# Kernel optimization log

Measured on AMD Instinct MI355X. Metric: run time of the kernel, lower is better.

Reference implementation:

```python
import jax, jax.numpy as jnp
import numpy as np
import math

VOCAB = 32000
D_MODEL = 512
N_LAYERS = 6
N_HEADS = 8
DIM_FF = 2048
B, L = 4, 2048
MAX_LEN = 5000
EPS = 1e-5


def _pos_encoding(max_len, d_model):
    pe = np.zeros((max_len, d_model), dtype=np.float32)
    pos = np.arange(max_len)[:, None].astype(np.float32)
    div = np.exp(np.arange(0, d_model, 2).astype(np.float32) * (-math.log(10000.0) / d_model))
    pe[:, 0::2] = np.sin(pos * div)
    pe[:, 1::2] = np.cos(pos * div)
    return jnp.asarray(pe)


def setup_inputs() -> dict:
    key = jax.random.key(0)
    ks = jax.random.split(key, 16)
    s = 0.02
    d, f, Ly = D_MODEL, DIM_FF, N_LAYERS
    inp = {
        "src": jax.random.randint(ks[0], (B, L), 0, VOCAB, dtype=jnp.int32),
        "embed": jax.random.normal(ks[1], (VOCAB, d), jnp.float32) * s,
        "pe": _pos_encoding(MAX_LEN, d),
        "Wq": jax.random.normal(ks[2], (Ly, d, d), jnp.float32) * s,
        "bq": jnp.zeros((Ly, d), jnp.float32),
        "Wk": jax.random.normal(ks[3], (Ly, d, d), jnp.float32) * s,
        "bk": jnp.zeros((Ly, d), jnp.float32),
        "Wv": jax.random.normal(ks[4], (Ly, d, d), jnp.float32) * s,
        "bv": jnp.zeros((Ly, d), jnp.float32),
        "Wo": jax.random.normal(ks[5], (Ly, d, d), jnp.float32) * s,
        "bo": jnp.zeros((Ly, d), jnp.float32),
        "W1": jax.random.normal(ks[6], (Ly, d, f), jnp.float32) * s,
        "b1": jnp.zeros((Ly, f), jnp.float32),
        "W2": jax.random.normal(ks[7], (Ly, f, d), jnp.float32) * s,
        "b2": jnp.zeros((Ly, d), jnp.float32),
        "g1": jnp.ones((Ly, d), jnp.float32),
        "be1": jnp.zeros((Ly, d), jnp.float32),
        "g2": jnp.ones((Ly, d), jnp.float32),
        "be2": jnp.zeros((Ly, d), jnp.float32),
    }
    return inp


def _layernorm(x, g, b):
    mu = jnp.mean(x, axis=-1, keepdims=True)
    var = jnp.mean((x - mu) ** 2, axis=-1, keepdims=True)
    return (x - mu) * jax.lax.rsqrt(var + EPS) * g + b


def _encoder(src, embed, pe, Wq, bq, Wk, bk, Wv, bv, Wo, bo, W1, b1, W2, b2, g1, be1, g2, be2):
    Bb, Ll = src.shape
    H = N_HEADS
    hd = D_MODEL // H
    x = embed[src] + pe[:Ll]  # [B, L, D]
    for i in range(Wq.shape[0]):
        # NOTE: faithful to the source: .view(B, H, L, hd) with NO transpose
        q = (x @ Wq[i] + bq[i]).reshape(Bb, H, Ll, hd)
        k = (x @ Wk[i] + bk[i]).reshape(Bb, H, Ll, hd)
        v = (x @ Wv[i] + bv[i]).reshape(Bb, H, Ll, hd)
        scores = jnp.einsum('bhqd,bhkd->bhqk', q, k) / math.sqrt(hd)
        w = jax.nn.softmax(scores, axis=-1)
        o = jnp.einsum('bhqk,bhkd->bhqd', w, v)
        o = o.transpose(0, 2, 1, 3).reshape(Bb, Ll, D_MODEL)
        o = o @ Wo[i] + bo[i]
        x = _layernorm(x + o, g1[i], be1[i])
        ff = jax.nn.relu(x @ W1[i] + b1[i]) @ W2[i] + b2[i]
        x = _layernorm(x + ff, g2[i], be2[i])
    return x


def reference(src, embed, pe, Wq, bq, Wk, bk, Wv, bv, Wo, bo, W1, b1, W2, b2, g1, be1, g2, be2):
    return _encoder(src, embed, pe, Wq, bq, Wk, bk, Wv, bv, Wo, bo, W1, b1, W2, b2, g1, be1, g2, be2)
```

## Files before the change

### kernel.cpp

```cpp
#include <hip/hip_runtime.h>
#include <hip/hip_bf16.h>

typedef unsigned short u16;
typedef __attribute__((ext_vector_type(8))) short bf16x8;
typedef __attribute__((ext_vector_type(2))) unsigned u32x2;
typedef __attribute__((ext_vector_type(4))) float f32x4;
typedef __attribute__((ext_vector_type(16))) float f32x16;

#define B_  4
#define L_  2048
#define D_  512
#define H_  8
#define HD_ 64
#define FF_ 2048
#define NL_ 6
#define M_  8192
#define MB_ 1048576ULL

#if __has_builtin(__builtin_amdgcn_exp2f)
#define EX2 __builtin_amdgcn_exp2f
#else
#define EX2 exp2f
#endif

__device__ __forceinline__ float b2f(u16 u) {
    unsigned v = ((unsigned)u) << 16;
    return __builtin_bit_cast(float, v);
}
__device__ __forceinline__ u16 f2b(float f) {
    unsigned u = __builtin_bit_cast(unsigned, f);
    unsigned r = u + 0x7FFFu + ((u >> 16) & 1u);
    return (u16)(r >> 16);
}
__device__ __forceinline__ unsigned pack2_bf16(float a, float b) {
    __hip_bfloat162 h = __float22bfloat162_rn(make_float2(a, b));
    unsigned u;
    __builtin_memcpy(&u, &h, 4);
    return u;
}
__device__ __forceinline__ float inp(const void* p, size_t i, int fp32) {
    return fp32 ? ((const float*)p)[i] : b2f(((const u16*)p)[i]);
}
__device__ __forceinline__ void gl2lds16(const void* g, void* l) {
    __builtin_amdgcn_global_load_lds(
        (const __attribute__((address_space(1))) void*)g,
        (__attribute__((address_space(3))) void*)l, 16, 0, 0);
}

__global__ void probe_k(const unsigned* __restrict__ g1, int* __restrict__ flag) {
    flag[0] = (g1[0] == 0x3F800000u) ? 1 : 0;
}

__global__ __launch_bounds__(256) void transpose_layer_k2(const void* __restrict__ Wq,
                                                          const void* __restrict__ Wk,
                                                          const void* __restrict__ Wv,
                                                          const void* __restrict__ Wo,
                                                          const void* __restrict__ W1,
                                                          const void* __restrict__ W2,
                                                          size_t wo, size_t wf,
                                                          u16* __restrict__ Wt,
                                                          const int* __restrict__ flag) {
    __shared__ u16 tile[32][33];
    int fp32 = flag[0];
    int bid = blockIdx.x;
    const void* in;
    size_t off;
    u16* out;
    int rows, cols, tx, ty;
    if (bid < 1024) {
        int which = bid >> 8;
        in = (which == 0) ? Wq : (which == 1) ? Wk : (which == 2) ? Wv : Wo;
        off = wo;
        out = Wt + (size_t)which * (512 * 512);
        rows = 512; cols = 512;
        int t = bid & 255; tx = t & 15; ty = t >> 4;
    } else if (bid < 2048) {
        in = W1; off = wf; out = Wt + 4 * (512 * 512);
        rows = 512; cols = 2048;
        int t = bid - 1024; tx = t & 63; ty = t >> 6;
    } else {
        in = W2; off = wf; out = Wt + 4 * (512 * 512) + 512 * 2048;
        rows = 2048; cols = 512;
        int t = bid - 2048; tx = t & 15; ty = t >> 4;
    }
    int c0 = tx * 32, r0 = ty * 32;
    int lx = threadIdx.x & 31, ly = threadIdx.x >> 5;
    #pragma unroll
    for (int i = ly; i < 32; i += 8)
        tile[i][lx] = f2b(inp(in, off + (size_t)(r0 + i) * cols + c0 + lx, fp32));
    __syncthreads();
    #pragma unroll
    for (int i = ly; i < 32; i += 8)
        out[(size_t)(c0 + i) * rows + r0 + lx] = tile[lx][i];
}

__global__ __launch_bounds__(256) void embed_k(const int* __restrict__ src,
                                               const void* __restrict__ embed,
                                               const void* __restrict__ pe,
                                               float* __restrict__ xf,
                                               u16* __restrict__ xb,
                                               const int* __restrict__ flag) {
    int fp32 = flag[0];
    int idx = blockIdx.x * 256 + threadIdx.x;
    int m = idx >> 9;
    int d = idx & 511;
    int tok = src[m];
    float v = inp(embed, (size_t)tok * D_ + d, fp32)
            + inp(pe, (size_t)(m & (L_ - 1)) * D_ + d, fp32);
    xf[idx] = v;
    xb[idx] = f2b(v);
}

template <int TM, int TN, int WM, int WN, int WRITE_BF16, int RELU>
__device__ __forceinline__ void gemm_core(const u16* __restrict__ A,
                                          const u16* __restrict__ Bt,
                                          int tnB, int tnC,
                                          const void* __restrict__ bias, size_t boff,
                                          float* __restrict__ Cf, u16* __restrict__ Cb,
                                          int N, int K, int kbeg, int kend,
                                          float cscale, int fp32, int use_bias) {
    constexpr int BK = 32;
    __shared__ u16 Asm[TM * BK];
    __shared__ u16 Bsm[TN * BK];
    int tm = blockIdx.y * TM;
    int tid = threadIdx.x;
    int wave = tid >> 6, lane = tid & 63, quad = lane >> 4, l16 = lane & 15;
    constexpr int NWN = TN / WN;
    int wm = (wave / NWN) * WM, wn = (wave % NWN) * WN;
    constexpr int FI = WM / 16, FJ = WN / 16;
    constexpr int CA = TM / 64;
    constexpr int CB = TN / 64;

    int arowl = (lane >> 2);
    int akc   = (lane & 3) * 8;

    f32x4 acc[FI][FJ];
    #pragma unroll
    for (int i = 0; i < FI; i++)
        #pragma unroll
        for (int j = 0; j < FJ; j++) { f32x4 z = {0.f, 0.f, 0.f, 0.f}; acc[i][j] = z; }

    for (int k0 = kbeg; k0 < kend; k0 += BK) {
        __syncthreads();
        #pragma unroll
        for (int c = 0; c < CA; c++) {
            int chunk = wave * CA + c;
            int row = chunk * 16 + arowl;
            gl2lds16(A + (size_t)(tm + row) * K + k0 + akc, &Asm[chunk * 16 * BK]);
        }
        #pragma unroll
        for (int c = 0; c < CB; c++) {
            int chunk = wave * CB + c;
            int row = chunk * 16 + arowl;
            gl2lds16(Bt + (size_t)(tnB + row) * K + k0 + akc, &Bsm[chunk * 16 * BK]);
        }
        __syncthreads();
        bf16x8 af[FI], bfr[FJ];
        #pragma unroll
        for (int i = 0; i < FI; i++)
            af[i] = *(bf16x8*)&Asm[(wm + i * 16 + l16) * BK + quad * 8];
        #pragma unroll
        for (int j = 0; j < FJ; j++)
            bfr[j] = *(bf16x8*)&Bsm[(wn + j * 16 + l16) * BK + quad * 8];
        #pragma unroll
        for (int i = 0; i < FI; i++)
            #pragma unroll
            for (int j = 0; j < FJ; j++)
                acc[i][j] = __builtin_amdgcn_mfma_f32_16x16x32_bf16(af[i], bfr[j], acc[i][j], 0, 0, 0);
    }

    #pragma unroll
    for (int i = 0; i < FI; i++) {
        int row = tm + wm + i * 16 + quad * 4;
        #pragma unroll
        for (int j = 0; j < FJ; j++) {
            int col = tnC + wn + j * 16 + l16;
            float bv = use_bias ? inp(bias, boff + col, fp32) : 0.f;
            #pragma unroll
            for (int r = 0; r < 4; r++) {
                float v = (acc[i][j][r] + bv) * cscale;
                if (RELU) v = v > 0.f ? v : 0.f;
                size_t idx = (size_t)(row + r) * N + col;
                if (WRITE_BF16) Cb[idx] = f2b(v);
                else            Cf[idx] = v;
            }
        }
    }
}

__global__ __launch_bounds__(256) void gemm_qkv(const u16* A, const u16* Wt,
                                                const void* bq, const void* bk, const void* bv,
                                                size_t boff, u16* Qb, u16* Kb, u16* Vb,
                                                int K, float qscale, const int* flag) {
    int tnB = blockIdx.x * 128;
    int mat = tnB >> 9;
    int tnC = tnB & 511;
    u16* Cb = (mat == 0) ? Qb : (mat == 1) ? Kb : Vb;
    const void* bias = (mat == 0) ? bq : (mat == 1) ? bk : bv;
    float sc = (mat == 0) ? qscale : 1.0f;
    gemm_core<128, 128, 64, 64, 1, 0>(A, Wt, tnB, tnC, bias, boff, nullptr, Cb, 512, K, 0, K, sc, flag[0], 1);
}
__global__ __launch_bounds__(256) void gemm128_b16_relu(const u16* A, const u16* Bt, const void* bias, size_t boff,
                                                        u16* Cb, int N, int K, const int* flag) {
    int tn = blockIdx.x * 128;
    gemm_core<128, 128, 64, 64, 1, 1>(A, Bt, tn, tn, bias, boff, nullptr, Cb, N, K, 0, K, 1.0f, flag[0], 1);
}
__global__ __launch_bounds__(256) void gemm64_f32_sk(const u16* A, const u16* Bt, const void* bias, size_t boff,
                                                     float* Cf, int N, int K, const int* flag) {
    int tn = blockIdx.x * 128;
    int z = blockIdx.z;
    int ks = K / gridDim.z;
    gemm_core<64, 128, 64, 32, 0, 0>(A, Bt, tn, tn, bias, boff, Cf + (size_t)z * M_ * 512, nullptr,
                                     N, K, z * ks, z * ks + ks, 1.0f, flag[0], z == 0);
}

__global__ __launch_bounds__(256) void vperm_k(const u16* __restrict__ in, u16* __restrict__ out) {
    __shared__ u16 tile[32][33];
    int bh = blockIdx.z;
    const u16* pin = in + (size_t)bh * (L_ * HD_);
    u16* pout = out + (size_t)bh * (L_ * HD_);
    int c0 = blockIdx.x * 32, r0 = blockIdx.y * 32;
    int lx = threadIdx.x & 31, ly = threadIdx.x >> 5;
    #pragma unroll
    for (int i = ly; i < 32; i += 8)
        tile[i][lx] = pin[(size_t)(r0 + i) * HD_ + c0 + lx];
    __syncthreads();
    #pragma unroll
    for (int i = ly; i < 32; i += 8)
        pout[(size_t)(c0 + i) * L_ + r0 + lx] = tile[lx][i];
}

__device__ __forceinline__ bf16x8 frag_from4(unsigned w0, unsigned w1, unsigned w2, unsigned w3) {
    union { unsigned u[4]; bf16x8 v; } t;
    t.u[0] = w0; t.u[1] = w1; t.u[2] = w2; t.u[3] = w3;
    return t.v;
}
__device__ __forceinline__ void lane32_swap(unsigned& x, unsigned& y, int hi) {
#if __has_builtin(__builtin_amdgcn_permlane32_swap)
    u32x2 r = __builtin_amdgcn_permlane32_swap(x, y, false, false);
    x = r[0]; y = r[1];
#else
    unsigned tx = (unsigned)__shfl_xor((int)x, 32, 64);
    unsigned ty = (unsigned)__shfl_xor((int)y, 32, 64);
    x = hi ? ty : x;
    y = hi ? y : tx;
#endif
}

__global__ __launch_bounds__(256, 4) void attn_k(const u16* __restrict__ Q,
                                                 const u16* __restrict__ K,
                                                 const u16* __restrict__ Vt,
                                                 u16* __restrict__ O) {
    constexpr int NT = L_ / 64;
    __shared__ u16 TILES[4][64 * 64];
    __shared__ float LsP[2][2][2][32];
    int qt = blockIdx.x;
    int bh = blockIdx.y;
    int b = bh >> 3, h = bh & 7;
    size_t hb = (size_t)bh * (L_ * HD_);
    int tid = threadIdx.x, wave = tid >> 6, lane = tid & 63, hi = lane >> 5, r32 = lane & 31;
    int wqq = wave >> 1, wk = wave & 1;

    const char* Kg = (const char*)(K + hb);
    const char* Vg = (const char*)(Vt + hb);

    int rsub = lane >> 3;
    int scol = (((lane & 7) ^ rsub) << 4);

    const u16* qp = Q + hb + (size_t)(qt * 64 + wqq * 32 + r32) * HD_ + hi * 8;
    bf16x8 qf[4];
    #pragma unroll
    for (int dc = 0; dc < 4; dc++) qf[dc] = *(const bf16x8*)(qp + dc * 16);

    #pragma unroll
    for (int c = 0; c < 2; c++) {
        int row = wave * 16 + c * 8 + rsub;
        gl2lds16(Kg + (size_t)row * (HD_ * 2) + scol, &TILES[0][(wave * 16 + c * 8) * 64]);
        gl2lds16(Vg + (size_t)row * (L_ * 2) + scol, &TILES[2][(wave * 16 + c * 8) * 64]);
    }

    f32x16 oac0, oac1;
    #pragma unroll
    for (int i = 0; i < 16; i++) { oac0[i] = 0.f; oac1[i] = 0.f; }
    float ls = 0.f;

    int krow = wk * 32 + r32;
    int ksw = (krow & 7) << 4;
    int vsw = (r32 & 7) << 4;

    int cur = 0;
    for (int kt = 0; kt < NT; kt++) {
        __syncthreads();
        if (kt + 1 < NT) {
            #pragma unroll
            for (int c = 0; c < 2; c++) {
                int row = wave * 16 + c * 8 + rsub;
                gl2lds16(Kg + (size_t)((kt + 1) * 64 + row) * (HD_ * 2) + scol,
                         &TILES[cur ^ 1][(wave * 16 + c * 8) * 64]);
                gl2lds16(Vg + (size_t)row * (L_ * 2) + (kt + 1) * 128 + scol,
                         &TILES[2 + (cur ^ 1)][(wave * 16 + c * 8) * 64]);
            }
        }

        const char* Kb = (const char*)&TILES[cur][0];
        const char* Vb = (const char*)&TILES[2 + cur][0];

        bf16x8 kf[4];
        #pragma unroll
        for (int dc = 0; dc < 4; dc++)
            kf[dc] = *(const bf16x8*)(Kb + krow * 128 + ((dc * 32 + hi * 16) ^ ksw));
        bf16x8 vf[4];
        vf[0] = *(const bf16x8*)(Vb + r32 * 128        + ((wk * 64 + hi * 16) ^ vsw));
        vf[1] = *(const bf16x8*)(Vb + r32 * 128        + ((wk * 64 + 32 + hi * 16) ^ vsw));
        vf[2] = *(const bf16x8*)(Vb + (32 + r32) * 128 + ((wk * 64 + hi * 16) ^ vsw));
        vf[3] = *(const bf16x8*)(Vb + (32 + r32) * 128 + ((wk * 64 + 32 + hi * 16) ^ vsw));

        f32x16 sac;
        #pragma unroll
        for (int i = 0; i < 16; i++) sac[i] = 0.f;
        __builtin_amdgcn_s_setprio(1);
        #pragma unroll
        for (int dc = 0; dc < 4; dc++)
            sac = __builtin_amdgcn_mfma_f32_32x32x16_bf16(kf[dc], qf[dc], sac, 0, 0, 0);
        __builtin_amdgcn_s_setprio(0);

        float p[16];
        #pragma unroll
        for (int r = 0; r < 16; r++) p[r] = EX2(sac[r]);
        {
            float a = (p[0] + p[1]) + (p[2] + p[3]);
            float c = (p[4] + p[5]) + (p[6] + p[7]);
            float e = (p[8] + p[9]) + (p[10] + p[11]);
            float g = (p[12] + p[13]) + (p[14] + p[15]);
            ls += (a + c) + (e + g);
        }
        bf16x8 pa[2];
        #pragma unroll
        for (int c = 0; c < 2; c++) {
            int rb = c * 8;
            unsigned a0 = pack2_bf16(p[rb + 0], p[rb + 1]);
            unsigned a1 = pack2_bf16(p[rb + 2], p[rb + 3]);
            unsigned a2 = pack2_bf16(p[rb + 4], p[rb + 5]);
            unsigned a3 = pack2_bf16(p[rb + 6], p[rb + 7]);
            lane32_swap(a0, a2, hi);
            lane32_swap(a1, a3, hi);
            pa[c] = frag_from4(a0, a1, a2, a3);
        }

        __builtin_amdgcn_s_setprio(1);
        oac0 = __builtin_amdgcn_mfma_f32_32x32x16_bf16(pa[0], vf[0], oac0, 0, 0, 0);
        oac1 = __builtin_amdgcn_mfma_f32_32x32x16_bf16(pa[0], vf[2], oac1, 0, 0, 0);
        oac0 = __builtin_amdgcn_mfma_f32_32x32x16_bf16(pa[1], vf[1], oac0, 0, 0, 0);
        oac1 = __builtin_amdgcn_mfma_f32_32x32x16_bf16(pa[1], vf[3], oac1, 0, 0, 0);
        __builtin_amdgcn_s_setprio(0);

        cur ^= 1;
    }

    __syncthreads();
    float* RedF = (float*)&TILES[0][0];
    LsP[wqq][wk][hi][r32] = ls;
    if (wk == 1) {
        #pragma unroll
        for (int r = 0; r < 16; r++) {
            RedF[(wqq * 64 + lane) * 33 + r]      = oac0[r];
            RedF[(wqq * 64 + lane) * 33 + 16 + r] = oac1[r];
        }
    }
    __syncthreads();
    if (wk == 0) {
        #pragma unroll
        for (int r = 0; r < 16; r++) {
            int qr = (r & 3) + 8 * (r >> 2) + 4 * hi;
            float den = LsP[wqq][0][0][qr] + LsP[wqq][0][1][qr]
                      + LsP[wqq][1][0][qr] + LsP[wqq][1][1][qr];
            float inv = 1.0f / fmaxf(den, 1e-30f);
            float v0 = (oac0[r] + RedF[(wqq * 64 + lane) * 33 + r]) * inv;
            float v1 = (oac1[r] + RedF[(wqq * 64 + lane) * 33 + 16 + r]) * inv;
            int qg = qt * 64 + wqq * 32 + qr;
            size_t ob = ((size_t)b * L_ + qg) * D_ + h * HD_;
            O[ob + r32]      = f2b(v0);
            O[ob + 32 + r32] = f2b(v1);
        }
    }
}

__global__ __launch_bounds__(256) void ln_k2(const float* resid,
                                             const float* __restrict__ delta0,
                                             const float* __restrict__ delta1,
                                             const void* __restrict__ g,
                                             const void* __restrict__ be, size_t goff,
                                             float* xf_out,
                                             void* __restrict__ out_raw,
                                             const int* __restrict__ flag,
                                             int two, int is_final) {
    int fp32 = flag[0];
    int row = blockIdx.x * 4 + (threadIdx.x >> 6);
    int lane = threadIdx.x & 63;
    const float* pr = resid + (size_t)row * D_;
    const float* pd0 = delta0 + (size_t)row * D_;
    const float* pd1 = delta1 + (size_t)row * D_;
    float u[8];
    float s = 0.f;
    #pragma unroll
    for (int i = 0; i < 8; i++) {
        int c = lane + i * 64;
        u[i] = pr[c] + pd0[c] + (two ? pd1[c] : 0.f);
        s += u[i];
    }
    #pragma unroll
    for (int d = 1; d < 64; d <<= 1) s += __shfl_xor(s, d);
    float mu = s * (1.0f / 512.0f);
    float vs = 0.f;
    #pragma unroll
    for (int i = 0; i < 8; i++) { float t = u[i] - mu; vs += t * t; }
    #pragma unroll
    for (int d = 1; d < 64; d <<= 1) vs += __shfl_xor(vs, d);
    float rstd = rsqrtf(vs * (1.0f / 512.0f) + 1e-5f);
    #pragma unroll
    for (int i = 0; i < 8; i++) {
        int c = lane + i * 64;
        float v = (u[i] - mu) * rstd * inp(g, goff + c, fp32) + inp(be, goff + c, fp32);
        xf_out[(size_t)row * D_ + c] = v;
        size_t oi = (size_t)row * D_ + c;
        if (is_final && fp32) ((float*)out_raw)[oi] = v;
        else                  ((u16*)out_raw)[oi]  = f2b(v);
    }
}

extern "C" void kernel_launch(void* const* d_in, const int* in_sizes, int n_in,
                              void* d_out, int out_size, void* d_ws, size_t ws_size,
                              hipStream_t stream) {
    (void)in_sizes; (void)n_in; (void)out_size;
    const int*  src   = (const int*)d_in[0];
    const void* embed = d_in[1];
    const void* pe    = d_in[2];
    const void* Wq = d_in[3];  const void* bq = d_in[4];
    const void* Wk = d_in[5];  const void* bk = d_in[6];
    const void* Wv = d_in[7];  const void* bv = d_in[8];
    const void* Wo = d_in[9];  const void* bo = d_in[10];
    const void* W1 = d_in[11]; const void* b1 = d_in[12];
    const void* W2 = d_in[13]; const void* b2 = d_in[14];
    const void* g1 = d_in[15]; const void* be1 = d_in[16];
    const void* g2 = d_in[17]; const void* be2 = d_in[18];

    int big = (ws_size >= 103 * MB_ + 64);
    char* ws = (char*)d_ws;
    float* xf  = (float*)(ws);
    u16*  xb   = (u16*)(ws + 16 * MB_);
    u16*  Qb   = (u16*)(ws + 24 * MB_);
    u16*  Kb   = (u16*)(ws + 32 * MB_);
    u16*  Vb   = (u16*)(ws + 40 * MB_);
    u16*  Vt   = (u16*)(ws + 48 * MB_);
    u16*  Ab   = (u16*)(ws + 56 * MB_);
    float* Pf0 = (float*)(ws + 24 * MB_);
    float* Pf1 = (float*)(ws + 40 * MB_);
    u16*  Hb   = (u16*)(ws + (big ? 64 : 40) * MB_);
    u16*  Wt   = (u16*)(ws + (big ? 96 : 72) * MB_);
    int*  flag = (int*)(ws + (big ? 102 : 78) * MB_);
    u16* Wot = Wt + 786432;
    u16* W1t = Wt + 1048576;
    u16* W2t = Wt + 2097152;

    const float QSCALE = 0.125f * 1.44269504f;

    probe_k<<<1, 1, 0, stream>>>((const unsigned*)g1, flag);
    embed_k<<<(M_ * D_) / 256, 256, 0, stream>>>(src, embed, pe, xf, xb, flag);

    for (int i = 0; i < NL_; i++) {
        size_t wo = (size_t)i * 512 * 512;
        size_t wf = (size_t)i * 512 * 2048;
        size_t vo = (size_t)i * 512;
        size_t fo = (size_t)i * 2048;
        transpose_layer_k2<<<3072, 256, 0, stream>>>(Wq, Wk, Wv, Wo, W1, W2, wo, wf, Wt, flag);

        gemm_qkv<<<dim3(12, 64), 256, 0, stream>>>(xb, Wt, bq, bk, bv, vo, Qb, Kb, Vb, 512, QSCALE, flag);
        vperm_k<<<dim3(2, 64, 32), 256, 0, stream>>>(Vb, Vt);
        attn_k<<<dim3(32, 32), 256, 0, stream>>>(Qb, Kb, Vt, Ab);
        gemm64_f32_sk<<<dim3(4, 128, 1), 256, 0, stream>>>(Ab, Wot, bo, vo, Pf0, 512, 512, flag);
        ln_k2<<<M_ / 4, 256, 0, stream>>>(xf, Pf0, Pf0, g1, be1, vo, xf, xb, flag, 0, 0);
        gemm128_b16_relu<<<dim3(16, 64), 256, 0, stream>>>(xb, W1t, b1, fo, Hb, 2048, 512, flag);
        if (big) gemm64_f32_sk<<<dim3(4, 128, 2), 256, 0, stream>>>(Hb, W2t, b2, vo, Pf0, 512, 2048, flag);
        else     gemm64_f32_sk<<<dim3(4, 128, 1), 256, 0, stream>>>(Hb, W2t, b2, vo, Pf0, 512, 2048, flag);
        void* out_raw = (i == NL_ - 1) ? d_out : (void*)xb;
        ln_k2<<<M_ / 4, 256, 0, stream>>>(xf, Pf0, Pf1, g2, be2, vo, xf, out_raw, flag, big ? 1 : 0, (i == NL_ - 1) ? 1 : 0);
    }
}
```

Before: 1.391 ms.

## Widen GEMM K-step to 64 and use 128-query attention blocks with 8 waves

The GEMM core now loads two 32-wide K slices per barrier pair, halving the number of __syncthreads per K loop at the cost of doubled LDS. The attention kernel grows to 512 threads covering 128 query rows per block, so each K/V tile staged in LDS is shared by twice as many queries and each wave loads half as many rows. Attention also gets a dedicated reduction buffer instead of reusing the tile memory, which raises LDS use and may lower occupancy.

```diff
diff --git a/kernel.cpp b/kernel.cpp
--- a/kernel.cpp
+++ b/kernel.cpp
@@ -120,8 +120,8 @@
                                           int N, int K, int kbeg, int kend,
                                           float cscale, int fp32, int use_bias) {
     constexpr int BK = 32;
-    __shared__ u16 Asm[TM * BK];
-    __shared__ u16 Bsm[TN * BK];
+    __shared__ u16 Asm[2][TM * BK];
+    __shared__ u16 Bsm[2][TN * BK];
     int tm = blockIdx.y * TM;
     int tid = threadIdx.x;
     int wave = tid >> 6, lane = tid & 63, quad = lane >> 4, l16 = lane & 15;
@@ -140,33 +140,40 @@
         #pragma unroll
         for (int j = 0; j < FJ; j++) { f32x4 z = {0.f, 0.f, 0.f, 0.f}; acc[i][j] = z; }
 
-    for (int k0 = kbeg; k0 < kend; k0 += BK) {
+    for (int k0 = kbeg; k0 < kend; k0 += 64) {
         __syncthreads();
         #pragma unroll
-        for (int c = 0; c < CA; c++) {
-            int chunk = wave * CA + c;
-            int row = chunk * 16 + arowl;
-            gl2lds16(A + (size_t)(tm + row) * K + k0 + akc, &Asm[chunk * 16 * BK]);
-        }
-        #pragma unroll
-        for (int c = 0; c < CB; c++) {
-            int chunk = wave * CB + c;
-            int row = chunk * 16 + arowl;
-            gl2lds16(Bt + (size_t)(tnB + row) * K + k0 + akc, &Bsm[chunk * 16 * BK]);
+        for (int half = 0; half < 2; half++) {
+            int kh = k0 + half * 32;
+            #pragma unroll
+            for (int c = 0; c < CA; c++) {
+                int chunk = wave * CA + c;
+                int row = chunk * 16 + arowl;
+                gl2lds16(A + (size_t)(tm + row) * K + kh + akc, &Asm[half][chunk * 16 * BK]);
+            }
+            #pragma unroll
+            for (int c = 0; c < CB; c++) {
+                int chunk = wave * CB + c;
+                int row = chunk * 16 + arowl;
+                gl2lds16(Bt + (size_t)(tnB + row) * K + kh + akc, &Bsm[half][chunk * 16 * BK]);
+            }
         }
         __syncthreads();
-        bf16x8 af[FI], bfr[FJ];
-        #pragma unroll
-        for (int i = 0; i < FI; i++)
-            af[i] = *(bf16x8*)&Asm[(wm + i * 16 + l16) * BK + quad * 8];
-        #pragma unroll
-        for (int j = 0; j < FJ; j++)
-            bfr[j] = *(bf16x8*)&Bsm[(wn + j * 16 + l16) * BK + quad * 8];
-        #pragma unroll
-        for (int i = 0; i < FI; i++)
+        #pragma unroll
+        for (int half = 0; half < 2; half++) {
+            bf16x8 af[FI], bfr[FJ];
+            #pragma unroll
+            for (int i = 0; i < FI; i++)
+                af[i] = *(bf16x8*)&Asm[half][(wm + i * 16 + l16) * BK + quad * 8];
             #pragma unroll
             for (int j = 0; j < FJ; j++)
-                acc[i][j] = __builtin_amdgcn_mfma_f32_16x16x32_bf16(af[i], bfr[j], acc[i][j], 0, 0, 0);
+                bfr[j] = *(bf16x8*)&Bsm[half][(wn + j * 16 + l16) * BK + quad * 8];
+            #pragma unroll
+            for (int i = 0; i < FI; i++)
+                #pragma unroll
+                for (int j = 0; j < FJ; j++)
+                    acc[i][j] = __builtin_amdgcn_mfma_f32_16x16x32_bf16(af[i], bfr[j], acc[i][j], 0, 0, 0);
+        }
     }
 
     #pragma unroll
@@ -247,13 +254,14 @@
 #endif
 }
 
-__global__ __launch_bounds__(256, 4) void attn_k(const u16* __restrict__ Q,
+__global__ __launch_bounds__(512, 4) void attn_k(const u16* __restrict__ Q,
                                                  const u16* __restrict__ K,
                                                  const u16* __restrict__ Vt,
                                                  u16* __restrict__ O) {
     constexpr int NT = L_ / 64;
     __shared__ u16 TILES[4][64 * 64];
-    __shared__ float LsP[2][2][2][32];
+    __shared__ float RedF[4][64][33];
+    __shared__ float LsP[4][2][2][32];
     int qt = blockIdx.x;
     int bh = blockIdx.y;
     int b = bh >> 3, h = bh & 7;
@@ -266,18 +274,15 @@
 
     int rsub = lane >> 3;
     int scol = (((lane & 7) ^ rsub) << 4);
-
-    const u16* qp = Q + hb + (size_t)(qt * 64 + wqq * 32 + r32) * HD_ + hi * 8;
+    int srow = wave * 8 + rsub;
+
+    const u16* qp = Q + hb + (size_t)(qt * 128 + wqq * 32 + r32) * HD_ + hi * 8;
     bf16x8 qf[4];
     #pragma unroll
     for (int dc = 0; dc < 4; dc++) qf[dc] = *(const bf16x8*)(qp + dc * 16);
 
-    #pragma unroll
-    for (int c = 0; c < 2; c++) {
-        int row = wave * 16 + c * 8 + rsub;
-        gl2lds16(Kg + (size_t)row * (HD_ * 2) + scol, &TILES[0][(wave * 16 + c * 8) * 64]);
-        gl2lds16(Vg + (size_t)row * (L_ * 2) + scol, &TILES[2][(wave * 16 + c * 8) * 64]);
-    }
+    gl2lds16(Kg + (size_t)srow * (HD_ * 2) + scol, &TILES[0][(wave * 8) * 64]);
+    gl2lds16(Vg + (size_t)srow * (L_ * 2) + scol, &TILES[2][(wave * 8) * 64]);
 
     f32x16 oac0, oac1;
     #pragma unroll
@@ -292,14 +297,10 @@
     for (int kt = 0; kt < NT; kt++) {
         __syncthreads();
         if (kt + 1 < NT) {
-            #pragma unroll
-            for (int c = 0; c < 2; c++) {
-                int row = wave * 16 + c * 8 + rsub;
-                gl2lds16(Kg + (size_t)((kt + 1) * 64 + row) * (HD_ * 2) + scol,
-                         &TILES[cur ^ 1][(wave * 16 + c * 8) * 64]);
-                gl2lds16(Vg + (size_t)row * (L_ * 2) + (kt + 1) * 128 + scol,
-                         &TILES[2 + (cur ^ 1)][(wave * 16 + c * 8) * 64]);
-            }
+            gl2lds16(Kg + (size_t)((kt + 1) * 64 + srow) * (HD_ * 2) + scol,
+                     &TILES[cur ^ 1][(wave * 8) * 64]);
+            gl2lds16(Vg + (size_t)srow * (L_ * 2) + (kt + 1) * 128 + scol,
+                     &TILES[2 + (cur ^ 1)][(wave * 8) * 64]);
         }
 
         const char* Kb = (const char*)&TILES[cur][0];
@@ -358,13 +359,12 @@
     }
 
     __syncthreads();
-    float* RedF = (float*)&TILES[0][0];
     LsP[wqq][wk][hi][r32] = ls;
     if (wk == 1) {
         #pragma unroll
         for (int r = 0; r < 16; r++) {
-            RedF[(wqq * 64 + lane) * 33 + r]      = oac0[r];
-            RedF[(wqq * 64 + lane) * 33 + 16 + r] = oac1[r];
+            RedF[wqq][lane][r]      = oac0[r];
+            RedF[wqq][lane][16 + r] = oac1[r];
         }
     }
     __syncthreads();
@@ -375,9 +375,9 @@
             float den = LsP[wqq][0][0][qr] + LsP[wqq][0][1][qr]
                       + LsP[wqq][1][0][qr] + LsP[wqq][1][1][qr];
             float inv = 1.0f / fmaxf(den, 1e-30f);
-            float v0 = (oac0[r] + RedF[(wqq * 64 + lane) * 33 + r]) * inv;
-            float v1 = (oac1[r] + RedF[(wqq * 64 + lane) * 33 + 16 + r]) * inv;
-            int qg = qt * 64 + wqq * 32 + qr;
+            float v0 = (oac0[r] + RedF[wqq][lane][r]) * inv;
+            float v1 = (oac1[r] + RedF[wqq][lane][16 + r]) * inv;
+            int qg = qt * 128 + wqq * 32 + qr;
             size_t ob = ((size_t)b * L_ + qg) * D_ + h * HD_;
             O[ob + r32]      = f2b(v0);
             O[ob + 32 + r32] = f2b(v1);
@@ -476,7 +476,7 @@
 
         gemm_qkv<<<dim3(12, 64), 256, 0, stream>>>(xb, Wt, bq, bk, bv, vo, Qb, Kb, Vb, 512, QSCALE, flag);
         vperm_k<<<dim3(2, 64, 32), 256, 0, stream>>>(Vb, Vt);
-        attn_k<<<dim3(32, 32), 256, 0, stream>>>(Qb, Kb, Vt, Ab);
+        attn_k<<<dim3(16, 32), 512, 0, stream>>>(Qb, Kb, Vt, Ab);
         gemm64_f32_sk<<<dim3(4, 128, 1), 256, 0, stream>>>(Ab, Wot, bo, vo, Pf0, 512, 512, flag);
         ln_k2<<<M_ / 4, 256, 0, stream>>>(xf, Pf0, Pf0, g1, be1, vo, xf, xb, flag, 0, 0);
         gemm128_b16_relu<<<dim3(16, 64), 256, 0, stream>>>(xb, W1t, b1, fo, Hb, 2048, 512, flag);
```

New measurement: 1.336 ms. 3.9% less time.
